# Optimization experiments

Measured on AMD Instinct MI355X. Metric: run time of the kernel, lower is better.

Reference implementation:

```python
import jax, jax.numpy as jnp
import numpy as np
import math

EMBED = 768
HEADS = 12
HEAD_DIM = EMBED // HEADS

def setup_inputs() -> dict:
    key = jax.random.key(0)
    ks = jax.random.split(key, 9)
    B, T, C = 32, 1024, EMBED
    s = 1.0 / math.sqrt(C)
    return {
        "hidden_states": jax.random.normal(ks[0], (B, T, C), dtype=jnp.float32),
        "q_w": jax.random.normal(ks[1], (C, C), dtype=jnp.float32) * s,
        "q_b": jnp.zeros((C,), dtype=jnp.float32),
        "k_w": jax.random.normal(ks[2], (C, C), dtype=jnp.float32) * s,
        "k_b": jnp.zeros((C,), dtype=jnp.float32),
        "v_w": jax.random.normal(ks[3], (C, C), dtype=jnp.float32) * s,
        "v_b": jnp.zeros((C,), dtype=jnp.float32),
        "o_w": jax.random.normal(ks[4], (C, C), dtype=jnp.float32) * s,
        "o_b": jnp.zeros((C,), dtype=jnp.float32),
    }

def reference(hidden_states, q_w, q_b, k_w, k_b, v_w, v_b, o_w, o_b):
    B, T, C = hidden_states.shape
    H, D = HEADS, C // HEADS
    # Linear: x @ W^T + b (torch nn.Linear convention); here weights stored (C, C)
    q = (hidden_states @ q_w.T + q_b).reshape(B, T, H, D).transpose(0, 2, 1, 3)
    k = (hidden_states @ k_w.T + k_b).reshape(B, T, H, D).transpose(0, 2, 1, 3)
    v = (hidden_states @ v_w.T + v_b).reshape(B, T, H, D).transpose(0, 2, 1, 3)
    scale = 1.0 / math.sqrt(D)
    scores = jnp.einsum("bhqd,bhkd->bhqk", q, k) * scale
    attn = jax.nn.softmax(scores, axis=-1)
    out = jnp.einsum("bhqk,bhkd->bhqd", attn, v)  # (B,H,T,D)
    out = out.transpose(0, 2, 1, 3).reshape(B, T, C)
    return out @ o_w.T + o_b
```

## Files before the change

kernel.cpp:

```cpp
#include <hip/hip_runtime.h>
#include <hip/hip_bf16.h>

#define B_ 32
#define T_ 1024
#define C_ 768
#define H_ 12
#define D_ 64
#define BT_ (B_*T_)
#define CC_ (C_*C_)

typedef __attribute__((ext_vector_type(4))) float f32x4;
typedef __attribute__((ext_vector_type(8))) short bf16x8;
typedef __attribute__((ext_vector_type(4))) short short4_t;
typedef unsigned short u16;
typedef unsigned int u32;

#define QSCALE 0.1803368801111244f

__device__ __forceinline__ float bf2f(u16 u){
  union { float f; unsigned int i; } v; v.i = ((unsigned int)u)<<16; return v.f;
}
__device__ __forceinline__ u16 f2bf(float f){
  union { float f; unsigned int i; } v; v.f = f;
  return (u16)((v.i + 0x7fffu + ((v.i>>16)&1u)) >> 16);
}
__device__ __forceinline__ u16 f2bf_fast(float f){
  union { float f; unsigned int i; } v; v.f = f;
  return (u16)((v.i + 0x8000u) >> 16);
}
__device__ __forceinline__ void split2(float f, u16& h, u16& l){
  h = f2bf(f);
  l = f2bf(f - bf2f(h));
}

__device__ __forceinline__ void gll16(const void* g, void* l){
  __builtin_amdgcn_global_load_lds(
      (const __attribute__((address_space(1))) u32*)g,
      (__attribute__((address_space(3))) u32*)l, 16, 0, 0);
}

__global__ void sentinel_kernel(float* out, int n){
  int i = blockIdx.x*blockDim.x + threadIdx.x;
  if (i < n) out[i] = 12345.0f;
}

__global__ void xquant_kernel(const float* __restrict__ x, u16* __restrict__ xb, int n8){
  int i = blockIdx.x*blockDim.x + threadIdx.x;
  int stride = gridDim.x*blockDim.x;
  for (; i < n8; i += stride) {
    f32x4 a = *(const f32x4*)(x + (size_t)i*8);
    f32x4 b = *(const f32x4*)(x + (size_t)i*8 + 4);
    bf16x8 o;
    #pragma unroll
    for (int j = 0; j < 4; ++j) { o[j] = (short)f2bf(a[j]); o[j+4] = (short)f2bf(b[j]); }
    *(bf16x8*)(xb + (size_t)i*8) = o;
  }
}

__global__ void wquant_kernel(const float* __restrict__ qw, const float* __restrict__ kw,
                              const float* __restrict__ vw, const float* __restrict__ ow,
                              u16* __restrict__ W3b, u16* __restrict__ Wohi,
                              u16* __restrict__ Wolo){
  int i = (blockIdx.x*blockDim.x + threadIdx.x)*4;
  if (i >= CC_) return;
  f32x4 q = *(const f32x4*)(qw+i);
  f32x4 k = *(const f32x4*)(kw+i);
  f32x4 v = *(const f32x4*)(vw+i);
  f32x4 o = *(const f32x4*)(ow+i);
  short4_t tq, tk, tv, th, tl;
  #pragma unroll
  for (int j = 0; j < 4; ++j) {
    tq[j] = (short)f2bf(q[j]);
    tk[j] = (short)f2bf(k[j]);
    tv[j] = (short)f2bf(v[j]);
    u16 hh, ll; split2(o[j], hh, ll);
    th[j] = (short)hh; tl[j] = (short)ll;
  }
  *(short4_t*)(W3b + i)          = tq;
  *(short4_t*)(W3b + CC_ + i)    = tk;
  *(short4_t*)(W3b + 2*CC_ + i)  = tv;
  *(short4_t*)(Wohi + i)         = th;
  *(short4_t*)(Wolo + i)         = tl;
}

template<int MODE>
__global__ __launch_bounds__(256,2)
void gemm_glds(const u16* __restrict__ Ab, const u16* __restrict__ Wb,
               const u16* __restrict__ Wlo_,
               const float* __restrict__ bq, const float* __restrict__ bk,
               const float* __restrict__ bv,
               u16* __restrict__ Qb, u16* __restrict__ Kb, u16* __restrict__ Vb,
               float* __restrict__ Out)
{
  __shared__ __align__(1024) u16 sA[128*64];
  __shared__ __align__(1024) u16 sB[128*64];
  __shared__ __align__(1024) u16 sBl[MODE==1 ? 128*64 : 8];
  const int tid = threadIdx.x;
  const int lane = tid & 63;
  const int l15 = lane & 15, l16 = lane >> 4;
  const int wave = tid >> 6;
  const int wr = wave >> 1, wc = wave & 1;

  const int bid = blockIdx.x;
  const int xcd = bid & 7;
  const int idx = bid >> 3;
  int z, nb, mloc;
  if (MODE == 0) { z = idx % 3; int r = idx / 3; nb = r % 6; mloc = r / 6; }
  else           { z = 0; nb = idx % 6; mloc = idx / 6; }
  const int m0 = (xcd*32 + mloc) * 128;
  const int n0 = nb * 128;
  const u16* W = (MODE==0) ? (Wb + (size_t)z*CC_) : Wb;
  const float* bias = (MODE==1) ? bq : (z==0 ? bq : (z==1 ? bk : bv));

  const int lrow = lane >> 3;
  const int cbyte = ((lane & 7) ^ lrow) << 4;

  f32x4 acc[4][4];
  #pragma unroll
  for (int i=0;i<4;++i)
    #pragma unroll
    for (int j=0;j<4;++j)
      acc[i][j] = (f32x4){0.f,0.f,0.f,0.f};

  for (int k0 = 0; k0 < C_; k0 += 64) {
    __syncthreads();
    #pragma unroll
    for (int sg = 0; sg < 4; ++sg) {
      int seg = wave*4 + sg;
      int row = seg*8 + lrow;
      gll16((const char*)(Ab + (size_t)(m0+row)*C_ + k0) + cbyte, sA + seg*512);
      gll16((const char*)(W  + (size_t)(n0+row)*C_ + k0) + cbyte, sB + seg*512);
      if (MODE == 1)
        gll16((const char*)(Wlo_ + (size_t)(n0+row)*C_ + k0) + cbyte, sBl + seg*512);
    }
    asm volatile("s_waitcnt vmcnt(0)" ::: "memory");
    __syncthreads();

    #pragma unroll
    for (int kc = 0; kc < 2; ++kc) {
      bf16x8 a[4], bh[4], bl[4];
      #pragma unroll
      for (int mf = 0; mf < 4; ++mf) {
        int row = wr*64 + mf*16 + l15;
        int off = (row<<7) + ((kc*64 + l16*16) ^ ((row&7)<<4));
        a[mf] = *(const bf16x8*)((const char*)sA + off);
      }
      #pragma unroll
      for (int nf = 0; nf < 4; ++nf) {
        int row = wc*64 + nf*16 + l15;
        int off = (row<<7) + ((kc*64 + l16*16) ^ ((row&7)<<4));
        bh[nf] = *(const bf16x8*)((const char*)sB + off);
        if (MODE == 1) bl[nf] = *(const bf16x8*)((const char*)sBl + off);
      }
      #pragma unroll
      for (int mf = 0; mf < 4; ++mf)
        #pragma unroll
        for (int nf = 0; nf < 4; ++nf) {
          acc[mf][nf] = __builtin_amdgcn_mfma_f32_16x16x32_bf16(a[mf], bh[nf], acc[mf][nf],0,0,0);
          if (MODE == 1)
            acc[mf][nf] = __builtin_amdgcn_mfma_f32_16x16x32_bf16(a[mf], bl[nf], acc[mf][nf],0,0,0);
        }
    }
  }

  #pragma unroll
  for (int mf = 0; mf < 4; ++mf) {
    #pragma unroll
    for (int nf = 0; nf < 4; ++nf) {
      int mgb = m0 + wr*64 + mf*16 + l16*4;
      int ng  = n0 + wc*64 + nf*16 + l15;
      float bv = bias[ng];
      if (MODE == 1) {
        #pragma unroll
        for (int r = 0; r < 4; ++r)
          Out[(size_t)(mgb+r)*C_ + ng] = acc[mf][nf][r] + bv;
      } else {
        int b = mgb >> 10, t0 = mgb & 1023;
        int h = ng >> 6, d = ng & 63;
        int bh_ = b*H_ + h;
        if (z == 2) {
          short4_t vh;
          #pragma unroll
          for (int r = 0; r < 4; ++r)
            vh[r] = (short)f2bf(acc[mf][nf][r] + bv);
          size_t idx2 = ((size_t)bh_*D_ + d)*T_ + t0;
          *(short4_t*)&Vb[idx2] = vh;
        } else {
          u16* dst = (z==0) ? Qb : Kb;
          float scale = (z==0) ? QSCALE : 1.0f;
          #pragma unroll
          for (int r = 0; r < 4; ++r) {
            size_t idx2 = ((size_t)bh_*T_ + (t0+r))*D_ + d;
            dst[idx2] = f2bf((acc[mf][nf][r] + bv) * scale);
          }
        }
      }
    }
  }
}

__global__ __launch_bounds__(256,2)
void attn_kernel(const u16* __restrict__ Qb, const u16* __restrict__ Kb,
                 const u16* __restrict__ Vb, u16* __restrict__ AOb)
{
  __shared__ __align__(16) u16 sK[64*64];
  __shared__ __align__(16) u16 sV[64*64];
  __shared__ __align__(16) u16 sP[4][16*64];
  const int tid = threadIdx.x;
  const int lane = tid & 63;
  const int l15 = lane & 15, l16 = lane >> 4;
  const int wave = tid >> 6;
  const int bid = blockIdx.x;
  const int sw  = (bid & 7) * 768 + (bid >> 3);
  const int bh  = sw >> 4;
  const int q0  = (sw & 15) * 64 + wave * 16;

  bf16x8 qh[2];
  #pragma unroll
  for (int kc = 0; kc < 2; ++kc)
    qh[kc] = *(const bf16x8*)(Qb + ((size_t)bh*T_ + q0 + l15)*D_ + kc*32 + l16*8);

  f32x4 o[4];
  #pragma unroll
  for (int i=0;i<4;++i) o[i] = (f32x4){0.f,0.f,0.f,0.f};
  float l_r[4] = {0.f,0.f,0.f,0.f};

  const size_t kbase = (size_t)bh * (T_*D_);
  const size_t vbase = (size_t)bh * (D_*T_);
  char* pb = (char*)sP[wave];

  for (int kt = 0; kt < T_/64; ++kt) {
    __syncthreads();
    #pragma unroll
    for (int iss = 0; iss < 2; ++iss) {
      int oo = (iss*256 + tid)*16;
      int row = oo >> 7;
      int colb = oo & 127;
      int dst = (row<<7) | (colb ^ ((row&7)<<4));
      const char* k_s = (const char*)(Kb + kbase + (size_t)(kt*64+row)*D_) + colb;
      const char* v_s = (const char*)(Vb + vbase + (size_t)row*T_ + kt*64) + colb;
      *(bf16x8*)((char*)sK + dst) = *(const bf16x8*)k_s;
      *(bf16x8*)((char*)sV + dst) = *(const bf16x8*)v_s;
    }
    __syncthreads();

    f32x4 s[4];
    #pragma unroll
    for (int nf = 0; nf < 4; ++nf) {
      s[nf] = (f32x4){0.f,0.f,0.f,0.f};
      #pragma unroll
      for (int kc = 0; kc < 2; ++kc) {
        int row = nf*16 + l15;
        int off = (row<<7) | (((kc*64) + l16*16) ^ ((row&7)<<4));
        bf16x8 kf = *(const bf16x8*)((const char*)sK + off);
        s[nf] = __builtin_amdgcn_mfma_f32_16x16x32_bf16(qh[kc], kf, s[nf],0,0,0);
      }
    }

    #pragma unroll
    for (int nf = 0; nf < 4; ++nf) {
      #pragma unroll
      for (int r = 0; r < 4; ++r) {
        float p = __builtin_amdgcn_exp2f(s[nf][r]);
        l_r[r] += p;
        int qr = l16*4 + r;
        int off = (qr<<7) | (((nf*16 + l15)<<1) ^ ((qr&7)<<4));
        *(u16*)(pb + off) = f2bf_fast(p);
      }
    }

    #pragma unroll
    for (int kc = 0; kc < 2; ++kc) {
      int offp = (l15<<7) | (((kc*64) + l16*16) ^ ((l15&7)<<4));
      bf16x8 pa = *(const bf16x8*)(pb + offp);
      #pragma unroll
      for (int df = 0; df < 4; ++df) {
        int row = df*16 + l15;
        int offv = (row<<7) | (((kc*64) + l16*16) ^ ((row&7)<<4));
        bf16x8 vf = *(const bf16x8*)((const char*)sV + offv);
        o[df] = __builtin_amdgcn_mfma_f32_16x16x32_bf16(pa, vf, o[df],0,0,0);
      }
    }
  }

  #pragma unroll
  for (int r = 0; r < 4; ++r) {
    float t = l_r[r];
    #pragma unroll
    for (int off = 1; off < 16; off <<= 1)
      t += __shfl_xor(t, off);
    l_r[r] = t;
  }

  const int b = bh / H_, h = bh % H_;
  #pragma unroll
  for (int r = 0; r < 4; ++r) {
    float inv = 1.0f / l_r[r];
    int t = q0 + l16*4 + r;
    size_t rowb = ((size_t)(b*T_ + t))*C_ + h*D_;
    #pragma unroll
    for (int df = 0; df < 4; ++df)
      AOb[rowb + df*16 + l15] = f2bf(o[df][r] * inv);
  }
}

extern "C" void kernel_launch(void* const* d_in, const int* in_sizes, int n_in,
                              void* d_out, int out_size, void* d_ws, size_t ws_size,
                              hipStream_t stream) {
  const float* X  = (const float*)d_in[0];
  const float* qw = (const float*)d_in[1];
  const float* qb = (const float*)d_in[2];
  const float* kw = (const float*)d_in[3];
  const float* kb = (const float*)d_in[4];
  const float* vw = (const float*)d_in[5];
  const float* vb = (const float*)d_in[6];
  const float* ow = (const float*)d_in[7];
  const float* ob = (const float*)d_in[8];
  float* out = (float*)d_out;

  const size_t SZ = (size_t)BT_*C_*sizeof(u16);
  const size_t NEED = 4*SZ + 5*(size_t)CC_*sizeof(u16);
  if (ws_size < NEED) {
    sentinel_kernel<<<(out_size+255)/256,256,0,stream>>>(out, out_size);
    return;
  }
  char* ws = (char*)d_ws;
  u16* Qb   = (u16*)(ws + 0*SZ);
  u16* Kb   = (u16*)(ws + 1*SZ);
  u16* Vb   = (u16*)(ws + 2*SZ);
  u16* AOb  = (u16*)(ws + 3*SZ);
  u16* W3b  = (u16*)(ws + 4*SZ);
  u16* Wohi = W3b + 3*(size_t)CC_;
  u16* Wolo = Wohi + (size_t)CC_;
  u16* Xb   = AOb;

  wquant_kernel<<<CC_/4/256,256,0,stream>>>(qw, kw, vw, ow, W3b, Wohi, Wolo);
  xquant_kernel<<<2048,256,0,stream>>>(X, Xb, BT_*C_/8);
  gemm_glds<0><<<4608,256,0,stream>>>(Xb, W3b, nullptr, qb, kb, vb,
      Qb, Kb, Vb, nullptr);
  attn_kernel<<<6144,256,0,stream>>>(Qb, Kb, Vb, AOb);
  gemm_glds<1><<<1536,256,0,stream>>>(AOb, Wohi, Wolo, ob, nullptr, nullptr,
      nullptr, nullptr, nullptr, out);
}
```

Baseline: 407.7 us.

## Double query rows per wave in attention and prefetch next K/V tile into registers

Each wave in the attention kernel now handles 32 query rows instead of 16, so a block covers 128 queries and the grid is halved. Every K and V fragment read from shared memory feeds two MFMAs, which halves K/V global and LDS traffic per query. The next K/V tile is also loaded into registers while the current tile is being computed, hiding global load latency. The cost is higher register pressure and a larger shared P buffer, which may reduce occupancy under the 256,2 launch bounds.

Measured after the change: 382.7 us. 6.1% less time.

```diff
diff --git a/kernel.cpp b/kernel.cpp
--- a/kernel.cpp
+++ b/kernel.cpp
@@ -205,103 +205,136 @@
 {
   __shared__ __align__(16) u16 sK[64*64];
   __shared__ __align__(16) u16 sV[64*64];
-  __shared__ __align__(16) u16 sP[4][16*64];
+  __shared__ __align__(16) u16 sP[4][32*64];
   const int tid = threadIdx.x;
   const int lane = tid & 63;
   const int l15 = lane & 15, l16 = lane >> 4;
   const int wave = tid >> 6;
   const int bid = blockIdx.x;
-  const int sw  = (bid & 7) * 768 + (bid >> 3);
-  const int bh  = sw >> 4;
-  const int q0  = (sw & 15) * 64 + wave * 16;
-
-  bf16x8 qh[2];
-  #pragma unroll
-  for (int kc = 0; kc < 2; ++kc)
-    qh[kc] = *(const bf16x8*)(Qb + ((size_t)bh*T_ + q0 + l15)*D_ + kc*32 + l16*8);
-
-  f32x4 o[4];
-  #pragma unroll
-  for (int i=0;i<4;++i) o[i] = (f32x4){0.f,0.f,0.f,0.f};
-  float l_r[4] = {0.f,0.f,0.f,0.f};
+  const int sw  = (bid & 7) * 384 + (bid >> 3);
+  const int bh  = sw >> 3;
+  const int q0  = (sw & 7) * 128 + wave * 32;
+
+  bf16x8 qh[2][2];
+  #pragma unroll
+  for (int mf = 0; mf < 2; ++mf)
+    #pragma unroll
+    for (int kc = 0; kc < 2; ++kc)
+      qh[mf][kc] = *(const bf16x8*)(Qb + ((size_t)bh*T_ + q0 + mf*16 + l15)*D_ + kc*32 + l16*8);
+
+  f32x4 o[2][4];
+  #pragma unroll
+  for (int mf = 0; mf < 2; ++mf)
+    #pragma unroll
+    for (int i = 0; i < 4; ++i) o[mf][i] = (f32x4){0.f,0.f,0.f,0.f};
+  float l_r[2][4] = {{0.f,0.f,0.f,0.f},{0.f,0.f,0.f,0.f}};
 
   const size_t kbase = (size_t)bh * (T_*D_);
   const size_t vbase = (size_t)bh * (D_*T_);
   char* pb = (char*)sP[wave];
 
+  int srow[2], sdst[2], scolb[2];
+  #pragma unroll
+  for (int iss = 0; iss < 2; ++iss) {
+    int oo = (iss*256 + tid)*16;
+    srow[iss]  = oo >> 7;
+    scolb[iss] = oo & 127;
+    sdst[iss]  = (srow[iss]<<7) | (scolb[iss] ^ ((srow[iss]&7)<<4));
+  }
+  bf16x8 kreg[2], vreg[2];
+  #pragma unroll
+  for (int iss = 0; iss < 2; ++iss) {
+    kreg[iss] = *(const bf16x8*)((const char*)(Kb + kbase + (size_t)srow[iss]*D_) + scolb[iss]);
+    vreg[iss] = *(const bf16x8*)((const char*)(Vb + vbase + (size_t)srow[iss]*T_) + scolb[iss]);
+  }
+
   for (int kt = 0; kt < T_/64; ++kt) {
     __syncthreads();
     #pragma unroll
     for (int iss = 0; iss < 2; ++iss) {
-      int oo = (iss*256 + tid)*16;
-      int row = oo >> 7;
-      int colb = oo & 127;
-      int dst = (row<<7) | (colb ^ ((row&7)<<4));
-      const char* k_s = (const char*)(Kb + kbase + (size_t)(kt*64+row)*D_) + colb;
-      const char* v_s = (const char*)(Vb + vbase + (size_t)row*T_ + kt*64) + colb;
-      *(bf16x8*)((char*)sK + dst) = *(const bf16x8*)k_s;
-      *(bf16x8*)((char*)sV + dst) = *(const bf16x8*)v_s;
+      *(bf16x8*)((char*)sK + sdst[iss]) = kreg[iss];
+      *(bf16x8*)((char*)sV + sdst[iss]) = vreg[iss];
+    }
+    if (kt + 1 < T_/64) {
+      #pragma unroll
+      for (int iss = 0; iss < 2; ++iss) {
+        kreg[iss] = *(const bf16x8*)((const char*)(Kb + kbase + (size_t)((kt+1)*64+srow[iss])*D_) + scolb[iss]);
+        vreg[iss] = *(const bf16x8*)((const char*)(Vb + vbase + (size_t)srow[iss]*T_ + (kt+1)*64) + scolb[iss]);
+      }
     }
     __syncthreads();
 
-    f32x4 s[4];
+    f32x4 s[2][4];
+    #pragma unroll
+    for (int mf = 0; mf < 2; ++mf)
+      #pragma unroll
+      for (int nf = 0; nf < 4; ++nf) s[mf][nf] = (f32x4){0.f,0.f,0.f,0.f};
     #pragma unroll
     for (int nf = 0; nf < 4; ++nf) {
-      s[nf] = (f32x4){0.f,0.f,0.f,0.f};
       #pragma unroll
       for (int kc = 0; kc < 2; ++kc) {
         int row = nf*16 + l15;
         int off = (row<<7) | (((kc*64) + l16*16) ^ ((row&7)<<4));
         bf16x8 kf = *(const bf16x8*)((const char*)sK + off);
-        s[nf] = __builtin_amdgcn_mfma_f32_16x16x32_bf16(qh[kc], kf, s[nf],0,0,0);
-      }
-    }
-
-    #pragma unroll
-    for (int nf = 0; nf < 4; ++nf) {
-      #pragma unroll
-      for (int r = 0; r < 4; ++r) {
-        float p = __builtin_amdgcn_exp2f(s[nf][r]);
-        l_r[r] += p;
-        int qr = l16*4 + r;
-        int off = (qr<<7) | (((nf*16 + l15)<<1) ^ ((qr&7)<<4));
-        *(u16*)(pb + off) = f2bf_fast(p);
-      }
-    }
+        s[0][nf] = __builtin_amdgcn_mfma_f32_16x16x32_bf16(qh[0][kc], kf, s[0][nf],0,0,0);
+        s[1][nf] = __builtin_amdgcn_mfma_f32_16x16x32_bf16(qh[1][kc], kf, s[1][nf],0,0,0);
+      }
+    }
+
+    #pragma unroll
+    for (int mf = 0; mf < 2; ++mf)
+      #pragma unroll
+      for (int nf = 0; nf < 4; ++nf)
+        #pragma unroll
+        for (int r = 0; r < 4; ++r) {
+          float p = __builtin_amdgcn_exp2f(s[mf][nf][r]);
+          l_r[mf][r] += p;
+          int qr = mf*16 + l16*4 + r;
+          int off = (qr<<7) | (((nf*16 + l15)<<1) ^ ((qr&7)<<4));
+          *(u16*)(pb + off) = f2bf_fast(p);
+        }
 
     #pragma unroll
     for (int kc = 0; kc < 2; ++kc) {
-      int offp = (l15<<7) | (((kc*64) + l16*16) ^ ((l15&7)<<4));
-      bf16x8 pa = *(const bf16x8*)(pb + offp);
+      int offp0 = (l15<<7) | (((kc*64) + l16*16) ^ ((l15&7)<<4));
+      int row1 = 16 + l15;
+      int offp1 = (row1<<7) | (((kc*64) + l16*16) ^ ((row1&7)<<4));
+      bf16x8 pa0 = *(const bf16x8*)(pb + offp0);
+      bf16x8 pa1 = *(const bf16x8*)(pb + offp1);
       #pragma unroll
       for (int df = 0; df < 4; ++df) {
         int row = df*16 + l15;
         int offv = (row<<7) | (((kc*64) + l16*16) ^ ((row&7)<<4));
         bf16x8 vf = *(const bf16x8*)((const char*)sV + offv);
-        o[df] = __builtin_amdgcn_mfma_f32_16x16x32_bf16(pa, vf, o[df],0,0,0);
-      }
-    }
-  }
-
-  #pragma unroll
-  for (int r = 0; r < 4; ++r) {
-    float t = l_r[r];
-    #pragma unroll
-    for (int off = 1; off < 16; off <<= 1)
-      t += __shfl_xor(t, off);
-    l_r[r] = t;
-  }
+        o[0][df] = __builtin_amdgcn_mfma_f32_16x16x32_bf16(pa0, vf, o[0][df],0,0,0);
+        o[1][df] = __builtin_amdgcn_mfma_f32_16x16x32_bf16(pa1, vf, o[1][df],0,0,0);
+      }
+    }
+  }
+
+  #pragma unroll
+  for (int mf = 0; mf < 2; ++mf)
+    #pragma unroll
+    for (int r = 0; r < 4; ++r) {
+      float t = l_r[mf][r];
+      #pragma unroll
+      for (int off = 1; off < 16; off <<= 1)
+        t += __shfl_xor(t, off);
+      l_r[mf][r] = t;
+    }
 
   const int b = bh / H_, h = bh % H_;
   #pragma unroll
-  for (int r = 0; r < 4; ++r) {
-    float inv = 1.0f / l_r[r];
-    int t = q0 + l16*4 + r;
-    size_t rowb = ((size_t)(b*T_ + t))*C_ + h*D_;
-    #pragma unroll
-    for (int df = 0; df < 4; ++df)
-      AOb[rowb + df*16 + l15] = f2bf(o[df][r] * inv);
-  }
+  for (int mf = 0; mf < 2; ++mf)
+    #pragma unroll
+    for (int r = 0; r < 4; ++r) {
+      float inv = 1.0f / l_r[mf][r];
+      int t = q0 + mf*16 + l16*4 + r;
+      size_t rowb = ((size_t)(b*T_ + t))*C_ + h*D_;
+      #pragma unroll
+      for (int df = 0; df < 4; ++df)
+        AOb[rowb + df*16 + l15] = f2bf(o[mf][df][r] * inv);
+    }
 }
 
 extern "C" void kernel_launch(void* const* d_in, const int* in_sizes, int n_in,
@@ -338,7 +371,7 @@
   xquant_kernel<<<2048,256,0,stream>>>(X, Xb, BT_*C_/8);
   gemm_glds<0><<<4608,256,0,stream>>>(Xb, W3b, nullptr, qb, kb, vb,
       Qb, Kb, Vb, nullptr);
-  attn_kernel<<<6144,256,0,stream>>>(Qb, Kb, Vb, AOb);
+  attn_kernel<<<3072,256,0,stream>>>(Qb, Kb, Vb, AOb);
   gemm_glds<1><<<1536,256,0,stream>>>(AOb, Wohi, Wolo, ob, nullptr, nullptr,
       nullptr, nullptr, nullptr, out);
 }
```
